# Performance work log

Hardware: AMD Instinct MI355X
Metric: run time of the kernel (lower is better)

Reference implementation:

```python
import math
import jax, jax.numpy as jnp
import numpy as np

PRED_LEN = 96
K = 32
LOW_FREQ = 1


def setup_inputs() -> dict:
    key = jax.random.key(0)
    x = jax.random.normal(key, (8, 512, 512), dtype=jnp.float32)
    return {"x": x}


def _fourier_forward(x):
    b, t, d = x.shape
    # rFFT over time axis (always fp32, matching torch autocast-disabled block)
    x_freq = jnp.fft.rfft(x.astype(jnp.float32), axis=1)  # (b, t//2+1, d) complex64
    freqs = jnp.fft.rfftfreq(t).astype(jnp.float32)
    if t % 2 == 0:
        x_freq = x_freq[:, LOW_FREQ:-1]
        f = freqs[LOW_FREQ:-1]
    else:
        x_freq = x_freq[:, LOW_FREQ:]
        f = freqs[LOW_FREQ:]
    n_freq = x_freq.shape[1]
    k = min(K, n_freq)

    # top-k |X(f)| independently per (batch, channel): move freq to last axis
    mag = jnp.transpose(jnp.abs(x_freq), (0, 2, 1))          # (b, d, f)
    _, idx = jax.lax.top_k(mag, k)                            # (b, d, k)
    x_freq_t = jnp.transpose(x_freq, (0, 2, 1))               # (b, d, f)
    x_sel = jnp.transpose(jnp.take_along_axis(x_freq_t, idx, axis=2), (0, 2, 1))  # (b, k, d)
    f_sel = jnp.transpose(f[idx], (0, 2, 1))[:, :, None, :]   # (b, k, 1, d)

    # extrapolate: add conjugate (negative) frequencies
    x_full = jnp.concatenate([x_sel, jnp.conj(x_sel)], axis=1)  # (b, 2k, d)
    f_full = jnp.concatenate([f_sel, -f_sel], axis=1)           # (b, 2k, 1, d)
    t_val = jnp.arange(t + PRED_LEN, dtype=jnp.float32)[None, None, :, None]  # (1,1,T,1)
    amp = (jnp.abs(x_full) / t)[:, :, None, :]                  # (b, 2k, 1, d)
    phase = jnp.angle(x_full)[:, :, None, :]                    # (b, 2k, 1, d)
    x_time = amp * jnp.cos(2.0 * math.pi * f_full * t_val + phase)  # (b, 2k, T, d)
    return jnp.sum(x_time, axis=1)                              # (b, t+pred_len, d)


def reference(x):
    return _fourier_forward(x)
```

## Files before the change

kernel.cpp:

```cpp
#include <hip/hip_runtime.h>
#include <math.h>

#define BATCH 8
#define TLEN  512
#define DDIM  512
#define TOUT  608
#define KSEL  32
#define DT    8

#define TWO_PI_OVER_512 0.0122718463030851562f
#define SC (2.0f / 512.0f)

typedef __attribute__((ext_vector_type(8))) short short8;
typedef __attribute__((ext_vector_type(4))) float f32x4;

#define BMT_OFF 0
#define WK_OFF  4194304

__device__ __forceinline__ unsigned short f2bf(float f) {
    unsigned u = __float_as_uint(f);
    return (unsigned short)((u + 0x7FFF + ((u >> 16) & 1)) >> 16);
}

__device__ __constant__ const float CC16[16] = {
     1.f,  0.92387953251128674f,  0.70710678118654752f,  0.38268343236508977f,
     0.f, -0.38268343236508977f, -0.70710678118654752f, -0.92387953251128674f,
    -1.f, -0.92387953251128674f, -0.70710678118654752f, -0.38268343236508977f,
     0.f,  0.38268343236508977f,  0.70710678118654752f,  0.92387953251128674f };
__device__ __constant__ const float SS16[16] = {
     0.f,  0.38268343236508977f,  0.70710678118654752f,  0.92387953251128674f,
     1.f,  0.92387953251128674f,  0.70710678118654752f,  0.38268343236508977f,
     0.f, -0.38268343236508977f, -0.70710678118654752f, -0.92387953251128674f,
    -1.f, -0.92387953251128674f, -0.70710678118654752f, -0.38268343236508977f };

__global__ __launch_bounds__(512, 4) void fft_topk_kernel(const float* __restrict__ x,
                                                          unsigned short* __restrict__ BmT,
                                                          unsigned short* __restrict__ Wk) {
    __shared__ float2 Xl[DT][257];
    __shared__ float  ysr[16 * 33 * 9];
    __shared__ float  ysi[16 * 33 * 9];
    __shared__ float2 tw[512];

    const int tid = threadIdx.x;
    const int bid = blockIdx.x;
    const int b   = bid >> 6;
    const int d0  = ((bid & 7) * 8 + ((bid >> 3) & 7)) * DT;

    {
        float s, c;
        sincosf((float)tid * TWO_PI_OVER_512, &s, &c);
        tw[tid] = make_float2(c, s);
    }

    {
        const int h   = tid >> 8;
        const int rem = tid & 255;
        const int aA  = rem >> 3;
        const int dA  = rem & 7;
        const float* xb = x + ((size_t)b * TLEN + aA) * DDIM + d0 + dA;
        float xv[16];
        #pragma unroll
        for (int c = 0; c < 16; ++c)
            xv[c] = xb[(size_t)c * 32 * DDIM];

        #pragma unroll
        for (int qn = 0; qn < 8; ++qn) {
            const int q = qn + 8 * h;
            float sr = 0.f, si = 0.f;
            #pragma unroll
            for (int c = 0; c < 16; ++c) {
                const int n = (c * q) & 15;
                sr = fmaf(xv[c],  CC16[n], sr);
                si = fmaf(xv[c], -SS16[n], si);
            }
            ysr[(q * 33 + aA) * 9 + dA] = sr;
            ysi[(q * 33 + aA) * 9 + dA] = si;
        }
    }
    __syncthreads();

    {
        const int ahalf = tid & 1;
        const int dB    = (tid >> 1) & 7;
        const int kk    = tid >> 4;
        const int qq    = kk & 15;

        float Pr, Pi;
        if (ahalf == 0) { Pr = 1.f; Pi = 0.f; }
        else {
            float2 w = tw[(16 * kk) & 511];
            Pr = w.x; Pi = -w.y;
        }
        const float2 w2 = tw[kk];
        const float stc = w2.x, sts = w2.y;

        float ar[8] = {}, ai[8] = {};
        #pragma unroll
        for (int aa = 0; aa < 16; ++aa) {
            const int arow = ahalf * 16 + aa;
            float Yr = ysr[(qq * 33 + arow) * 9 + dB];
            float Yi = ysi[(qq * 33 + arow) * 9 + dB];
            float zr = Yr * Pr - Yi * Pi;
            float zi = Yr * Pi + Yi * Pr;
            #pragma unroll
            for (int u = 0; u < 8; ++u) {
                const int n = (aa * u) & 15;
                ar[u] = fmaf(zr, CC16[n], fmaf(zi,  SS16[n], ar[u]));
                ai[u] = fmaf(zi, CC16[n], fmaf(-zr, SS16[n], ai[u]));
            }
            float npr = fmaf(Pr, stc,  Pi * sts);
            Pi        = fmaf(Pi, stc, -Pr * sts);
            Pr        = npr;
        }

        #pragma unroll
        for (int u = 0; u < 8; ++u) {
            ar[u] += __shfl_xor(ar[u], 1);
            ai[u] += __shfl_xor(ai[u], 1);
        }
        #pragma unroll
        for (int v = 0; v < 4; ++v) {
            const int u = ahalf * 4 + v;
            Xl[dB][kk + 32 * u] = make_float2(ar[u], ai[u]);
        }
    }
    __syncthreads();

    if (tid < 256) {
        float2 w = tw[(bid * tid) & 511];
        unsigned val = (unsigned)f2bf(w.x * SC) | ((unsigned)f2bf(-w.y * SC) << 16);
        *(unsigned*)&Wk[((size_t)bid << 9) + 2 * tid] = val;
    }

    {
        const int l  = tid & 63;
        const int dd = tid >> 6;
        const unsigned long long below = ((unsigned long long)1 << l) - 1;

        float zr[4], zi[4];
        unsigned vb[4];
        int mm[4];
        #pragma unroll
        for (int s = 0; s < 4; ++s) {
            int m = 1 + l + 64 * s;
            mm[s] = m;
            if (m <= 255) {
                float2 z = Xl[dd][m];
                zr[s] = z.x; zi[s] = z.y;
                vb[s] = __float_as_uint(fmaf(z.x, z.x, z.y * z.y));
            } else { zr[s] = 0.f; zi[s] = 0.f; vb[s] = 0u; }
        }

        unsigned tau = 0;
        for (int bit = 30; bit >= 0; --bit) {
            unsigned cand = tau | (1u << bit);
            int cnt = __popcll(__ballot(vb[0] >= cand))
                    + __popcll(__ballot(vb[1] >= cand))
                    + __popcll(__ballot(vb[2] >= cand))
                    + __popcll(__ballot(vb[3] >= cand));
            if (cnt >= KSEL) tau = cand;
        }

        unsigned long long beq[4];
        int cgt = 0;
        #pragma unroll
        for (int s = 0; s < 4; ++s) {
            beq[s] = __ballot(vb[s] == tau);
            cgt += __popcll(__ballot(vb[s] > tau));
        }
        const int need = KSEL - cgt;

        unsigned short* Brow = BmT + ((size_t)(b * DDIM + d0 + dd) << 9);
        int be = 0;
        #pragma unroll
        for (int s = 0; s < 4; ++s) {
            bool keep = (vb[s] > tau);
            if (vb[s] == tau) {
                int r = be + __popcll(beq[s] & below);
                keep = (r < need);
            }
            be += __popcll(beq[s]);
            unsigned val = keep ? ((unsigned)f2bf(zr[s]) | ((unsigned)f2bf(zi[s]) << 16)) : 0u;
            int mi = mm[s] & 255;
            *(unsigned*)(Brow + 2 * mi) = val;
        }
    }
}

__global__ __launch_bounds__(512, 4) void gemm_kernel(const unsigned short* __restrict__ Wk,
                                                      const unsigned short* __restrict__ BmT,
                                                      float* __restrict__ out) {
    __shared__ unsigned short Al[64][72];
    __shared__ unsigned short Bl[64][72];

    const int tid = threadIdx.x;
    const int bid = blockIdx.x;
    const int bt  = bid >> 6;
    const int b   = (bid >> 3) & 7;
    const int bd  = bid & 7;

    const int wid  = tid >> 6;
    const int l    = tid & 63;
    const int wm   = wid & 3;
    const int wn   = wid >> 2;
    const int lrow = l & 15;
    const int lk8  = (l >> 4) * 8;

    const int srow = tid >> 3;
    const int soff = (tid & 7) * 8;

    const unsigned short* Wrow = Wk  + (size_t)(bt * 64 + srow) * 512 + soff;
    const unsigned short* Brow = BmT + ((size_t)(b * DDIM + bd * 64 + srow)) * 512 + soff;

    f32x4 acc0 = {0.f, 0.f, 0.f, 0.f};
    f32x4 acc1 = {0.f, 0.f, 0.f, 0.f};

    for (int kc = 0; kc < 512; kc += 64) {
        uint4 av = *(const uint4*)(Wrow + kc);
        uint4 bv = *(const uint4*)(Brow + kc);
        __syncthreads();
        *(uint4*)&Al[srow][soff] = av;
        *(uint4*)&Bl[srow][soff] = bv;
        __syncthreads();

        #pragma unroll
        for (int ks = 0; ks < 2; ++ks) {
            short8 af  = *(const short8*)&Al[wm * 16 + lrow][ks * 32 + lk8];
            short8 bf0 = *(const short8*)&Bl[wn * 32 + lrow][ks * 32 + lk8];
            short8 bf1 = *(const short8*)&Bl[wn * 32 + 16 + lrow][ks * 32 + lk8];
            acc0 = __builtin_amdgcn_mfma_f32_16x16x32_bf16(af, bf0, acc0, 0, 0, 0);
            acc1 = __builtin_amdgcn_mfma_f32_16x16x32_bf16(af, bf1, acc1, 0, 0, 0);
        }
    }

    const int tg = bt * 64 + wm * 16 + (l >> 4) * 4;
    const int dg = bd * 64 + wn * 32 + (l & 15);
    float* ob = out + (size_t)b * TOUT * DDIM;
    #pragma unroll
    for (int r = 0; r < 4; ++r) {
        const int t = tg + r;
        ob[(size_t)t * DDIM + dg]      = acc0[r];
        ob[(size_t)t * DDIM + dg + 16] = acc1[r];
        if (t < 96) {
            ob[(size_t)(t + 512) * DDIM + dg]      = acc0[r];
            ob[(size_t)(t + 512) * DDIM + dg + 16] = acc1[r];
        }
    }
}

extern "C" void kernel_launch(void* const* d_in, const int* in_sizes, int n_in,
                              void* d_out, int out_size, void* d_ws, size_t ws_size,
                              hipStream_t stream) {
    const float* x   = (const float*)d_in[0];
    float*       out = (float*)d_out;
    unsigned short* BmT = (unsigned short*)((char*)d_ws + BMT_OFF);
    unsigned short* Wk  = (unsigned short*)((char*)d_ws + WK_OFF);

    fft_topk_kernel<<<BATCH * 64, 512, 0, stream>>>(x, BmT, Wk);
    gemm_kernel<<<BATCH * 64, 512, 0, stream>>>(Wk, BmT, out);
}
```

Measured before the change: 27.15 us.

## Fuse FFT/top-k and GEMM into one kernel with inter-block flag sync

Merges the FFT+top-k kernel and the bf16 MFMA GEMM into a single launch. Each block first runs its FFT/top-k slice and publishes a release flag, then spins on acquire flags for the eight producer blocks it depends on before running its GEMM tile. The twiddle (Wk) matrix is no longer written to global memory; it is generated from the shared twiddle table inside the GEMM loop. This removes a kernel launch boundary and the Wk round trip. In exchange it depends on all 512 blocks being resident at once to avoid deadlock. The flags are never reset between calls, so a later call can pass the wait on stale flags and read BmT before it is rewritten.

```diff
diff --git a/kernel.cpp b/kernel.cpp
--- a/kernel.cpp
+++ b/kernel.cpp
@@ -10,12 +10,13 @@
 
 #define TWO_PI_OVER_512 0.0122718463030851562f
 #define SC (2.0f / 512.0f)
+#define MAGIC 0x5F3C0D1Eu
 
 typedef __attribute__((ext_vector_type(8))) short short8;
 typedef __attribute__((ext_vector_type(4))) float f32x4;
 
-#define BMT_OFF 0
-#define WK_OFF  4194304
+#define BMT_OFF  0
+#define FLAG_OFF 4194304
 
 __device__ __forceinline__ unsigned short f2bf(float f) {
     unsigned u = __float_as_uint(f);
@@ -33,217 +34,235 @@
      0.f, -0.38268343236508977f, -0.70710678118654752f, -0.92387953251128674f,
     -1.f, -0.92387953251128674f, -0.70710678118654752f, -0.38268343236508977f };
 
-__global__ __launch_bounds__(512, 4) void fft_topk_kernel(const float* __restrict__ x,
-                                                          unsigned short* __restrict__ BmT,
-                                                          unsigned short* __restrict__ Wk) {
-    __shared__ float2 Xl[DT][257];
-    __shared__ float  ysr[16 * 33 * 9];
-    __shared__ float  ysi[16 * 33 * 9];
-    __shared__ float2 tw[512];
+__global__ __launch_bounds__(512, 4) void fourier_fused(const float* __restrict__ x,
+                                                        unsigned short* __restrict__ BmT,
+                                                        unsigned* __restrict__ flags,
+                                                        float* __restrict__ out) {
+    __shared__ __align__(16) unsigned char smem[58560];
+    float2* Xl  = (float2*)smem;
+    float*  ysr = (float*)(smem + 16448);
+    float*  ysi = (float*)(smem + 35456);
+    float2* tw  = (float2*)(smem + 54464);
+    unsigned short* Al = (unsigned short*)smem;
+    unsigned short* Bl = (unsigned short*)(smem + 9216);
 
     const int tid = threadIdx.x;
     const int bid = blockIdx.x;
-    const int b   = bid >> 6;
-    const int d0  = ((bid & 7) * 8 + ((bid >> 3) & 7)) * DT;
 
     {
-        float s, c;
-        sincosf((float)tid * TWO_PI_OVER_512, &s, &c);
-        tw[tid] = make_float2(c, s);
+        const int b  = bid >> 6;
+        const int d0 = ((bid & 7) * 8 + ((bid >> 3) & 7)) * DT;
+
+        {
+            float s, c;
+            sincosf((float)tid * TWO_PI_OVER_512, &s, &c);
+            tw[tid] = make_float2(c, s);
+        }
+
+        {
+            const int h   = tid >> 8;
+            const int rem = tid & 255;
+            const int aA  = rem >> 3;
+            const int dA  = rem & 7;
+            const float* xb = x + ((size_t)b * TLEN + aA) * DDIM + d0 + dA;
+            float xv[16];
+            #pragma unroll
+            for (int c = 0; c < 16; ++c)
+                xv[c] = xb[(size_t)c * 32 * DDIM];
+
+            #pragma unroll
+            for (int qn = 0; qn < 8; ++qn) {
+                const int q = qn + 8 * h;
+                float sr = 0.f, si = 0.f;
+                #pragma unroll
+                for (int c = 0; c < 16; ++c) {
+                    const int n = (c * q) & 15;
+                    sr = fmaf(xv[c],  CC16[n], sr);
+                    si = fmaf(xv[c], -SS16[n], si);
+                }
+                ysr[(q * 33 + aA) * 9 + dA] = sr;
+                ysi[(q * 33 + aA) * 9 + dA] = si;
+            }
+        }
+        __syncthreads();
+
+        {
+            const int ahalf = tid & 1;
+            const int dB    = (tid >> 1) & 7;
+            const int kk    = tid >> 4;
+            const int qq    = kk & 15;
+
+            float Pr, Pi;
+            if (ahalf == 0) { Pr = 1.f; Pi = 0.f; }
+            else {
+                float2 w = tw[(16 * kk) & 511];
+                Pr = w.x; Pi = -w.y;
+            }
+            const float2 w2 = tw[kk];
+            const float stc = w2.x, sts = w2.y;
+
+            float ar[8] = {}, ai[8] = {};
+            #pragma unroll
+            for (int aa = 0; aa < 16; ++aa) {
+                const int arow = ahalf * 16 + aa;
+                float Yr = ysr[(qq * 33 + arow) * 9 + dB];
+                float Yi = ysi[(qq * 33 + arow) * 9 + dB];
+                float zr = Yr * Pr - Yi * Pi;
+                float zi = Yr * Pi + Yi * Pr;
+                #pragma unroll
+                for (int u = 0; u < 8; ++u) {
+                    const int n = (aa * u) & 15;
+                    ar[u] = fmaf(zr, CC16[n], fmaf(zi,  SS16[n], ar[u]));
+                    ai[u] = fmaf(zi, CC16[n], fmaf(-zr, SS16[n], ai[u]));
+                }
+                float npr = fmaf(Pr, stc,  Pi * sts);
+                Pi        = fmaf(Pi, stc, -Pr * sts);
+                Pr        = npr;
+            }
+
+            #pragma unroll
+            for (int u = 0; u < 8; ++u) {
+                ar[u] += __shfl_xor(ar[u], 1);
+                ai[u] += __shfl_xor(ai[u], 1);
+            }
+            #pragma unroll
+            for (int v = 0; v < 4; ++v) {
+                const int u = ahalf * 4 + v;
+                Xl[dB * 257 + kk + 32 * u] = make_float2(ar[u], ai[u]);
+            }
+        }
+        __syncthreads();
+
+        {
+            const int l  = tid & 63;
+            const int dd = tid >> 6;
+            const unsigned long long below = ((unsigned long long)1 << l) - 1;
+
+            float zr[4], zi[4];
+            unsigned vb[4];
+            int mm[4];
+            #pragma unroll
+            for (int s = 0; s < 4; ++s) {
+                int m = 1 + l + 64 * s;
+                mm[s] = m;
+                if (m <= 255) {
+                    float2 z = Xl[dd * 257 + m];
+                    zr[s] = z.x; zi[s] = z.y;
+                    vb[s] = __float_as_uint(fmaf(z.x, z.x, z.y * z.y));
+                } else { zr[s] = 0.f; zi[s] = 0.f; vb[s] = 0u; }
+            }
+
+            unsigned tau = 0;
+            for (int bit = 30; bit >= 0; --bit) {
+                unsigned cand = tau | (1u << bit);
+                int cnt = __popcll(__ballot(vb[0] >= cand))
+                        + __popcll(__ballot(vb[1] >= cand))
+                        + __popcll(__ballot(vb[2] >= cand))
+                        + __popcll(__ballot(vb[3] >= cand));
+                if (cnt >= KSEL) tau = cand;
+            }
+
+            unsigned long long beq[4];
+            int cgt = 0;
+            #pragma unroll
+            for (int s = 0; s < 4; ++s) {
+                beq[s] = __ballot(vb[s] == tau);
+                cgt += __popcll(__ballot(vb[s] > tau));
+            }
+            const int need = KSEL - cgt;
+
+            unsigned short* Brow = BmT + ((size_t)(b * DDIM + d0 + dd) << 9);
+            int be = 0;
+            #pragma unroll
+            for (int s = 0; s < 4; ++s) {
+                bool keep = (vb[s] > tau);
+                if (vb[s] == tau) {
+                    int r = be + __popcll(beq[s] & below);
+                    keep = (r < need);
+                }
+                be += __popcll(beq[s]);
+                unsigned val = keep ? ((unsigned)f2bf(zr[s]) | ((unsigned)f2bf(zi[s]) << 16)) : 0u;
+                int mi = mm[s] & 255;
+                *(unsigned*)(Brow + 2 * mi) = val;
+            }
+        }
+        __syncthreads();
+
+        if (tid == 0) {
+            __hip_atomic_store(&flags[((b * 8 + (bid & 7)) * 8) + ((bid >> 3) & 7)],
+                               MAGIC, __ATOMIC_RELEASE, __HIP_MEMORY_SCOPE_AGENT);
+        }
     }
 
     {
-        const int h   = tid >> 8;
-        const int rem = tid & 255;
-        const int aA  = rem >> 3;
-        const int dA  = rem & 7;
-        const float* xb = x + ((size_t)b * TLEN + aA) * DDIM + d0 + dA;
-        float xv[16];
+        const int bt = bid >> 6;
+        const int b  = (bid >> 3) & 7;
+        const int bd = bid & 7;
+
+        if (tid < 8) {
+            unsigned* f = flags + (b * 8 + bd) * 8;
+            while (__hip_atomic_load(&f[tid], __ATOMIC_ACQUIRE,
+                                     __HIP_MEMORY_SCOPE_AGENT) != MAGIC)
+                __builtin_amdgcn_s_sleep(2);
+        }
+        __syncthreads();
+
+        const int wid  = tid >> 6;
+        const int l    = tid & 63;
+        const int wm   = wid & 3;
+        const int wn   = wid >> 2;
+        const int lrow = l & 15;
+        const int lk8  = (l >> 4) * 8;
+
+        const int srow = tid >> 3;
+        const int soff = (tid & 7) * 8;
+        const int trow = bt * 64 + srow;
+
+        const unsigned short* Brow = BmT + ((size_t)(b * DDIM + bd * 64 + srow)) * 512 + soff;
+
+        f32x4 acc0 = {0.f, 0.f, 0.f, 0.f};
+        f32x4 acc1 = {0.f, 0.f, 0.f, 0.f};
+
+        for (int kc = 0; kc < 512; kc += 64) {
+            uint4 bv = *(const uint4*)(Brow + kc);
+            uint4 av;
+            {
+                const int m0 = (kc + soff) >> 1;
+                unsigned r[4];
+                #pragma unroll
+                for (int j = 0; j < 4; ++j) {
+                    float2 w = tw[(trow * (m0 + j)) & 511];
+                    r[j] = (unsigned)f2bf(w.x * SC) | ((unsigned)f2bf(-w.y * SC) << 16);
+                }
+                av.x = r[0]; av.y = r[1]; av.z = r[2]; av.w = r[3];
+            }
+            __syncthreads();
+            *(uint4*)&Al[srow * 72 + soff] = av;
+            *(uint4*)&Bl[srow * 72 + soff] = bv;
+            __syncthreads();
+
+            #pragma unroll
+            for (int ks = 0; ks < 2; ++ks) {
+                short8 af  = *(const short8*)&Al[(wm * 16 + lrow) * 72 + ks * 32 + lk8];
+                short8 bf0 = *(const short8*)&Bl[(wn * 32 + lrow) * 72 + ks * 32 + lk8];
+                short8 bf1 = *(const short8*)&Bl[(wn * 32 + 16 + lrow) * 72 + ks * 32 + lk8];
+                acc0 = __builtin_amdgcn_mfma_f32_16x16x32_bf16(af, bf0, acc0, 0, 0, 0);
+                acc1 = __builtin_amdgcn_mfma_f32_16x16x32_bf16(af, bf1, acc1, 0, 0, 0);
+            }
+        }
+
+        const int tg = bt * 64 + wm * 16 + (l >> 4) * 4;
+        const int dg = bd * 64 + wn * 32 + (l & 15);
+        float* ob = out + (size_t)b * TOUT * DDIM;
         #pragma unroll
-        for (int c = 0; c < 16; ++c)
-            xv[c] = xb[(size_t)c * 32 * DDIM];
-
-        #pragma unroll
-        for (int qn = 0; qn < 8; ++qn) {
-            const int q = qn + 8 * h;
-            float sr = 0.f, si = 0.f;
-            #pragma unroll
-            for (int c = 0; c < 16; ++c) {
-                const int n = (c * q) & 15;
-                sr = fmaf(xv[c],  CC16[n], sr);
-                si = fmaf(xv[c], -SS16[n], si);
-            }
-            ysr[(q * 33 + aA) * 9 + dA] = sr;
-            ysi[(q * 33 + aA) * 9 + dA] = si;
-        }
-    }
-    __syncthreads();
-
-    {
-        const int ahalf = tid & 1;
-        const int dB    = (tid >> 1) & 7;
-        const int kk    = tid >> 4;
-        const int qq    = kk & 15;
-
-        float Pr, Pi;
-        if (ahalf == 0) { Pr = 1.f; Pi = 0.f; }
-        else {
-            float2 w = tw[(16 * kk) & 511];
-            Pr = w.x; Pi = -w.y;
-        }
-        const float2 w2 = tw[kk];
-        const float stc = w2.x, sts = w2.y;
-
-        float ar[8] = {}, ai[8] = {};
-        #pragma unroll
-        for (int aa = 0; aa < 16; ++aa) {
-            const int arow = ahalf * 16 + aa;
-            float Yr = ysr[(qq * 33 + arow) * 9 + dB];
-            float Yi = ysi[(qq * 33 + arow) * 9 + dB];
-            float zr = Yr * Pr - Yi * Pi;
-            float zi = Yr * Pi + Yi * Pr;
-            #pragma unroll
-            for (int u = 0; u < 8; ++u) {
-                const int n = (aa * u) & 15;
-                ar[u] = fmaf(zr, CC16[n], fmaf(zi,  SS16[n], ar[u]));
-                ai[u] = fmaf(zi, CC16[n], fmaf(-zr, SS16[n], ai[u]));
-            }
-            float npr = fmaf(Pr, stc,  Pi * sts);
-            Pi        = fmaf(Pi, stc, -Pr * sts);
-            Pr        = npr;
-        }
-
-        #pragma unroll
-        for (int u = 0; u < 8; ++u) {
-            ar[u] += __shfl_xor(ar[u], 1);
-            ai[u] += __shfl_xor(ai[u], 1);
-        }
-        #pragma unroll
-        for (int v = 0; v < 4; ++v) {
-            const int u = ahalf * 4 + v;
-            Xl[dB][kk + 32 * u] = make_float2(ar[u], ai[u]);
-        }
-    }
-    __syncthreads();
-
-    if (tid < 256) {
-        float2 w = tw[(bid * tid) & 511];
-        unsigned val = (unsigned)f2bf(w.x * SC) | ((unsigned)f2bf(-w.y * SC) << 16);
-        *(unsigned*)&Wk[((size_t)bid << 9) + 2 * tid] = val;
-    }
-
-    {
-        const int l  = tid & 63;
-        const int dd = tid >> 6;
-        const unsigned long long below = ((unsigned long long)1 << l) - 1;
-
-        float zr[4], zi[4];
-        unsigned vb[4];
-        int mm[4];
-        #pragma unroll
-        for (int s = 0; s < 4; ++s) {
-            int m = 1 + l + 64 * s;
-            mm[s] = m;
-            if (m <= 255) {
-                float2 z = Xl[dd][m];
-                zr[s] = z.x; zi[s] = z.y;
-                vb[s] = __float_as_uint(fmaf(z.x, z.x, z.y * z.y));
-            } else { zr[s] = 0.f; zi[s] = 0.f; vb[s] = 0u; }
-        }
-
-        unsigned tau = 0;
-        for (int bit = 30; bit >= 0; --bit) {
-            unsigned cand = tau | (1u << bit);
-            int cnt = __popcll(__ballot(vb[0] >= cand))
-                    + __popcll(__ballot(vb[1] >= cand))
-                    + __popcll(__ballot(vb[2] >= cand))
-                    + __popcll(__ballot(vb[3] >= cand));
-            if (cnt >= KSEL) tau = cand;
-        }
-
-        unsigned long long beq[4];
-        int cgt = 0;
-        #pragma unroll
-        for (int s = 0; s < 4; ++s) {
-            beq[s] = __ballot(vb[s] == tau);
-            cgt += __popcll(__ballot(vb[s] > tau));
-        }
-        const int need = KSEL - cgt;
-
-        unsigned short* Brow = BmT + ((size_t)(b * DDIM + d0 + dd) << 9);
-        int be = 0;
-        #pragma unroll
-        for (int s = 0; s < 4; ++s) {
-            bool keep = (vb[s] > tau);
-            if (vb[s] == tau) {
-                int r = be + __popcll(beq[s] & below);
-                keep = (r < need);
-            }
-            be += __popcll(beq[s]);
-            unsigned val = keep ? ((unsigned)f2bf(zr[s]) | ((unsigned)f2bf(zi[s]) << 16)) : 0u;
-            int mi = mm[s] & 255;
-            *(unsigned*)(Brow + 2 * mi) = val;
-        }
-    }
-}
-
-__global__ __launch_bounds__(512, 4) void gemm_kernel(const unsigned short* __restrict__ Wk,
-                                                      const unsigned short* __restrict__ BmT,
-                                                      float* __restrict__ out) {
-    __shared__ unsigned short Al[64][72];
-    __shared__ unsigned short Bl[64][72];
-
-    const int tid = threadIdx.x;
-    const int bid = blockIdx.x;
-    const int bt  = bid >> 6;
-    const int b   = (bid >> 3) & 7;
-    const int bd  = bid & 7;
-
-    const int wid  = tid >> 6;
-    const int l    = tid & 63;
-    const int wm   = wid & 3;
-    const int wn   = wid >> 2;
-    const int lrow = l & 15;
-    const int lk8  = (l >> 4) * 8;
-
-    const int srow = tid >> 3;
-    const int soff = (tid & 7) * 8;
-
-    const unsigned short* Wrow = Wk  + (size_t)(bt * 64 + srow) * 512 + soff;
-    const unsigned short* Brow = BmT + ((size_t)(b * DDIM + bd * 64 + srow)) * 512 + soff;
-
-    f32x4 acc0 = {0.f, 0.f, 0.f, 0.f};
-    f32x4 acc1 = {0.f, 0.f, 0.f, 0.f};
-
-    for (int kc = 0; kc < 512; kc += 64) {
-        uint4 av = *(const uint4*)(Wrow + kc);
-        uint4 bv = *(const uint4*)(Brow + kc);
-        __syncthreads();
-        *(uint4*)&Al[srow][soff] = av;
-        *(uint4*)&Bl[srow][soff] = bv;
-        __syncthreads();
-
-        #pragma unroll
-        for (int ks = 0; ks < 2; ++ks) {
-            short8 af  = *(const short8*)&Al[wm * 16 + lrow][ks * 32 + lk8];
-            short8 bf0 = *(const short8*)&Bl[wn * 32 + lrow][ks * 32 + lk8];
-            short8 bf1 = *(const short8*)&Bl[wn * 32 + 16 + lrow][ks * 32 + lk8];
-            acc0 = __builtin_amdgcn_mfma_f32_16x16x32_bf16(af, bf0, acc0, 0, 0, 0);
-            acc1 = __builtin_amdgcn_mfma_f32_16x16x32_bf16(af, bf1, acc1, 0, 0, 0);
-        }
-    }
-
-    const int tg = bt * 64 + wm * 16 + (l >> 4) * 4;
-    const int dg = bd * 64 + wn * 32 + (l & 15);
-    float* ob = out + (size_t)b * TOUT * DDIM;
-    #pragma unroll
-    for (int r = 0; r < 4; ++r) {
-        const int t = tg + r;
-        ob[(size_t)t * DDIM + dg]      = acc0[r];
-        ob[(size_t)t * DDIM + dg + 16] = acc1[r];
-        if (t < 96) {
-            ob[(size_t)(t + 512) * DDIM + dg]      = acc0[r];
-            ob[(size_t)(t + 512) * DDIM + dg + 16] = acc1[r];
+        for (int r = 0; r < 4; ++r) {
+            const int t = tg + r;
+            ob[(size_t)t * DDIM + dg]      = acc0[r];
+            ob[(size_t)t * DDIM + dg + 16] = acc1[r];
+            if (t < 96) {
+                ob[(size_t)(t + 512) * DDIM + dg]      = acc0[r];
+                ob[(size_t)(t + 512) * DDIM + dg + 16] = acc1[r];
+            }
         }
     }
 }
@@ -253,9 +272,8 @@
                               hipStream_t stream) {
     const float* x   = (const float*)d_in[0];
     float*       out = (float*)d_out;
-    unsigned short* BmT = (unsigned short*)((char*)d_ws + BMT_OFF);
-    unsigned short* Wk  = (unsigned short*)((char*)d_ws + WK_OFF);
-
-    fft_topk_kernel<<<BATCH * 64, 512, 0, stream>>>(x, BmT, Wk);
-    gemm_kernel<<<BATCH * 64, 512, 0, stream>>>(Wk, BmT, out);
+    unsigned short* BmT   = (unsigned short*)((char*)d_ws + BMT_OFF);
+    unsigned*       flags = (unsigned*)((char*)d_ws + FLAG_OFF);
+
+    fourier_fused<<<512, 512, 0, stream>>>(x, BmT, flags, out);
 }
```

After: 39.87 us. +46.8%, slower.

## Prefetch next GEMM K-tile into registers, widen tile, and use direct twiddle lookups

Applied to the files above, without the earlier changes.

The GEMM kernel now stages 128-wide K chunks instead of 64, so there are half as many barrier pairs. It also issues the global loads for the next chunk before the MFMA work on the current one, overlapping memory latency with compute. Separately, the DFT stage preloads the Y values from shared memory and reads each twiddle directly from the table instead of advancing a serial complex-rotation recurrence. This removes the dependency chain and rounding drift, at the cost of more registers and more table reads.

```diff
diff --git a/kernel.cpp b/kernel.cpp
--- a/kernel.cpp
+++ b/kernel.cpp
@@ -85,32 +85,32 @@
         const int kk    = tid >> 4;
         const int qq    = kk & 15;
 
-        float Pr, Pi;
-        if (ahalf == 0) { Pr = 1.f; Pi = 0.f; }
-        else {
-            float2 w = tw[(16 * kk) & 511];
-            Pr = w.x; Pi = -w.y;
-        }
-        const float2 w2 = tw[kk];
-        const float stc = w2.x, sts = w2.y;
-
-        float ar[8] = {}, ai[8] = {};
+        const int ybase = (qq * 33 + ahalf * 16) * 9 + dB;
+        float Yr_[16], Yi_[16], Pr_[16], Pi_[16];
+        #pragma unroll
+        for (int aa = 0; aa < 16; ++aa) {
+            Yr_[aa] = ysr[ybase + aa * 9];
+            Yi_[aa] = ysi[ybase + aa * 9];
+        }
         #pragma unroll
         for (int aa = 0; aa < 16; ++aa) {
             const int arow = ahalf * 16 + aa;
-            float Yr = ysr[(qq * 33 + arow) * 9 + dB];
-            float Yi = ysi[(qq * 33 + arow) * 9 + dB];
-            float zr = Yr * Pr - Yi * Pi;
-            float zi = Yr * Pi + Yi * Pr;
+            float2 w = tw[(arow * kk) & 511];
+            Pr_[aa] = w.x;
+            Pi_[aa] = -w.y;
+        }
+
+        float ar[8] = {}, ai[8] = {};
+        #pragma unroll
+        for (int aa = 0; aa < 16; ++aa) {
+            float zr = Yr_[aa] * Pr_[aa] - Yi_[aa] * Pi_[aa];
+            float zi = Yr_[aa] * Pi_[aa] + Yi_[aa] * Pr_[aa];
             #pragma unroll
             for (int u = 0; u < 8; ++u) {
                 const int n = (aa * u) & 15;
                 ar[u] = fmaf(zr, CC16[n], fmaf(zi,  SS16[n], ar[u]));
                 ai[u] = fmaf(zi, CC16[n], fmaf(-zr, SS16[n], ai[u]));
             }
-            float npr = fmaf(Pr, stc,  Pi * sts);
-            Pi        = fmaf(Pi, stc, -Pr * sts);
-            Pr        = npr;
         }
 
         #pragma unroll
@@ -190,8 +190,8 @@
 __global__ __launch_bounds__(512, 4) void gemm_kernel(const unsigned short* __restrict__ Wk,
                                                       const unsigned short* __restrict__ BmT,
                                                       float* __restrict__ out) {
-    __shared__ unsigned short Al[64][72];
-    __shared__ unsigned short Bl[64][72];
+    __shared__ unsigned short Al[64][136];
+    __shared__ unsigned short Bl[64][136];
 
     const int tid = threadIdx.x;
     const int bid = blockIdx.x;
@@ -215,16 +215,28 @@
     f32x4 acc0 = {0.f, 0.f, 0.f, 0.f};
     f32x4 acc1 = {0.f, 0.f, 0.f, 0.f};
 
-    for (int kc = 0; kc < 512; kc += 64) {
-        uint4 av = *(const uint4*)(Wrow + kc);
-        uint4 bv = *(const uint4*)(Brow + kc);
+    uint4 av0 = *(const uint4*)(Wrow);
+    uint4 av1 = *(const uint4*)(Wrow + 64);
+    uint4 bv0 = *(const uint4*)(Brow);
+    uint4 bv1 = *(const uint4*)(Brow + 64);
+
+    for (int kc = 0; kc < 512; kc += 128) {
         __syncthreads();
-        *(uint4*)&Al[srow][soff] = av;
-        *(uint4*)&Bl[srow][soff] = bv;
+        *(uint4*)&Al[srow][soff]      = av0;
+        *(uint4*)&Al[srow][soff + 64] = av1;
+        *(uint4*)&Bl[srow][soff]      = bv0;
+        *(uint4*)&Bl[srow][soff + 64] = bv1;
         __syncthreads();
 
-        #pragma unroll
-        for (int ks = 0; ks < 2; ++ks) {
+        if (kc + 128 < 512) {
+            av0 = *(const uint4*)(Wrow + kc + 128);
+            av1 = *(const uint4*)(Wrow + kc + 192);
+            bv0 = *(const uint4*)(Brow + kc + 128);
+            bv1 = *(const uint4*)(Brow + kc + 192);
+        }
+
+        #pragma unroll
+        for (int ks = 0; ks < 4; ++ks) {
             short8 af  = *(const short8*)&Al[wm * 16 + lrow][ks * 32 + lk8];
             short8 bf0 = *(const short8*)&Bl[wn * 32 + lrow][ks * 32 + lk8];
             short8 bf1 = *(const short8*)&Bl[wn * 32 + 16 + lrow][ks * 32 + lk8];
```

Result: no change. 26.63 us (-1.9%).
